# Optimization experiments

Hardware: AMD Instinct MI355X
Metric: run time of the kernel (lower is better)

Reference implementation:

```python
import jax, jax.numpy as jnp
import numpy as np

T, B, D, H = 512, 64, 512, 1024


def setup_inputs() -> dict:
    key = jax.random.key(0)
    ks = jax.random.split(key, 4)
    scale = 1.0 / np.sqrt(D + H)
    return {
        "x": jax.random.normal(ks[0], (T, B, D), dtype=jnp.float32),
        "h0": jnp.zeros((B, H), dtype=jnp.float32),
        "Wz": jax.random.normal(ks[1], (H, D + H), dtype=jnp.float32) * scale,
        "bz": jnp.zeros((H,), dtype=jnp.float32),
        "Wr": jax.random.normal(ks[2], (H, D + H), dtype=jnp.float32) * scale,
        "br": jnp.zeros((H,), dtype=jnp.float32),
        "Wc": jax.random.normal(ks[3], (H, D + H), dtype=jnp.float32) * scale,
        "bc": jnp.zeros((H,), dtype=jnp.float32),
    }


def reference(x, h0, Wz, bz, Wr, br, Wc, bc):
    # x: [T, B, D], h0: [B, H]; weights follow torch Linear layout [out, in].
    def step(h, xt):
        xh = jnp.concatenate([xt, h], axis=-1)           # [B, D+H]
        z = jax.nn.sigmoid(xh @ Wz.T + bz)               # update gate [B, H]
        r = jax.nn.sigmoid(xh @ Wr.T + br)               # reset gate  [B, H]
        xrh = jnp.concatenate([xt, r * h], axis=-1)      # [B, D+H]
        hcand = jnp.tanh(xrh @ Wc.T + bc)                # candidate   [B, H]
        h_new = (1.0 - z) * h + z * hcand
        return h_new, h_new

    _, hist = jax.lax.scan(step, h0, x)                  # hist: [T, B, H]
    return hist
```

## Files before the change

kernel.cpp:

```cpp
#include <hip/hip_runtime.h>
#include <hip/hip_bf16.h>


typedef __attribute__((ext_vector_type(8))) short bf16x8;
typedef __attribute__((ext_vector_type(4))) float f32x4;

#define NWG 128
#define TSTEPS 512

static __device__ __forceinline__ float sigmoidf_fast(float x) {
    return 1.0f / (1.0f + __expf(-x));
}

static __device__ __forceinline__ unsigned short float_to_bf16bits(float f) {
    __hip_bfloat16 b = __float2bfloat16(f);
    unsigned short us;
    __builtin_memcpy(&us, &b, 2);
    return us;
}

static __device__ __forceinline__ void store_coh_u16(void* p, unsigned short v) {
    unsigned vv = v;
    asm volatile("global_store_short %0, %1, off sc0 sc1"
                 :: "v"(p), "v"(vv) : "memory");
}
static __device__ __forceinline__ void store_coh_u32(unsigned* p, unsigned v) {
    asm volatile("global_store_dword %0, %1, off sc0 sc1"
                 :: "v"(p), "v"(v) : "memory");
}

__global__ __launch_bounds__(256) void k_convert_weights(
    const float* __restrict__ Wz, const float* __restrict__ Wr,
    const float* __restrict__ Wc,
    __hip_bfloat16* __restrict__ Wzr, __hip_bfloat16* __restrict__ Wcb)
{
    const long long NW = 1024LL * 1536LL;
    const long long stride = (long long)gridDim.x * blockDim.x;
    for (long long i = (long long)blockIdx.x * blockDim.x + threadIdx.x;
         i < 3 * NW; i += stride) {
        if (i < NW)            Wzr[i] = __float2bfloat16(Wz[i]);
        else if (i < 2 * NW)   Wzr[i] = __float2bfloat16(Wr[i - NW]);
        else                   Wcb[i - 2 * NW] = __float2bfloat16(Wc[i - 2 * NW]);
    }
}

__global__ __launch_bounds__(256) void k_convert_x(
    const float* __restrict__ x, __hip_bfloat16* __restrict__ xb)
{
    const long long N = 512LL * 64LL * 512LL;
    const long long stride = (long long)gridDim.x * blockDim.x;
    for (long long i = (long long)blockIdx.x * blockDim.x + threadIdx.x;
         i < N; i += stride)
        xb[i] = __float2bfloat16(x[i]);
}

__global__ __launch_bounds__(256) void k_init_h(
    const float* __restrict__ h0, __hip_bfloat16* __restrict__ hb)
{
    int i = blockIdx.x * blockDim.x + threadIdx.x;
    hb[i] = __float2bfloat16(h0[i]);
}

__global__ __launch_bounds__(256, 1) void k_gru_persistent(
    const __hip_bfloat16* __restrict__ xb,
    const float* __restrict__ h0,
    __hip_bfloat16* __restrict__ hb_,
    const __hip_bfloat16* __restrict__ Wzr,
    const __hip_bfloat16* __restrict__ Wcb,
    const float* __restrict__ bz, const float* __restrict__ br,
    const float* __restrict__ bc,
    __hip_bfloat16* __restrict__ sb_,
    float* __restrict__ out,
    unsigned* __restrict__ flags)
{
    __shared__ short w1z[64 * 32 * 8];
    __shared__ short w1r[64 * 32 * 8];
    __shared__ short w2c[64 * 32 * 8];
    __shared__ f32x4 red[2][2][64];

    short* hb = (short*)hb_;
    short* sb = (short*)sb_;

    const int g = blockIdx.x;
    const int lane = threadIdx.x & 63;
    const int wave = threadIdx.x >> 6;
    const int r15 = lane & 15;
    const int q = lane >> 4;
    const int kk = q << 3;

    const int dom = g & 3;
    const int wgid = g >> 2;
    const int c0 = wgid * 32;
    const int mt = dom * 16;
    const int tile = wave & 1;
    const int kh = wave >> 1;
    const int jcol = c0 + tile * 16 + r15;
    const int mb = mt + (q << 2);
    const bool owner = (kh == 0);

    unsigned* myline = flags + (dom * 32 + wgid) * 32;
    const unsigned* pollflag = flags + (dom * 32 + (lane & 31)) * 32;

    for (int c = threadIdx.x; c < 64 * 32; c += 256) {
        int row = c & 31, blk = c >> 5;
        bf16x8 vz = *(const bf16x8*)((const short*)Wzr +
                                     (long long)(c0 + row) * 1536 + blk * 8);
        bf16x8 vr = *(const bf16x8*)((const short*)Wzr +
                                     (long long)(1024 + c0 + row) * 1536 + blk * 8);
        bf16x8 vc = *(const bf16x8*)((const short*)Wcb +
                                     (long long)(c0 + row) * 1536 + blk * 8);
        *(bf16x8*)(w1z + (blk * 32 + row) * 8) = vz;
        *(bf16x8*)(w1r + (blk * 32 + row) * 8) = vr;
        *(bf16x8*)(w2c + (blk * 32 + row) * 8) = vc;
    }

    bf16x8 wzh[16], wrh[16], wcs[16];
#pragma unroll
    for (int i = 0; i < 16; ++i) {
        int bk = 64 + kh * 64 + i * 4 + q;
        wzh[i] = *(const bf16x8*)((const short*)Wzr +
                                  (long long)jcol * 1536 + bk * 8);
        wrh[i] = *(const bf16x8*)((const short*)Wzr +
                                  (long long)(1024 + jcol) * 1536 + bk * 8);
        wcs[i] = *(const bf16x8*)((const short*)Wcb +
                                  (long long)jcol * 1536 + bk * 8);
    }

    const float biasZ = bz[jcol];
    const float biasR = br[jcol];
    const float biasC = bc[jcol];

    float hreg[4];
    if (owner) {
#pragma unroll
        for (int v = 0; v < 4; ++v)
            hreg[v] = h0[(mb + v) * 1024 + jcol];
    }
    __syncthreads();

    float zreg[4] = {0.f, 0.f, 0.f, 0.f};

    bf16x8 xc[8];
    {
        const short* Ax0 = (const short*)xb + (mt + r15) * 512 + kh * 256 + kk;
#pragma unroll
        for (int i = 0; i < 8; ++i)
            xc[i] = *(const bf16x8*)(Ax0 + i * 32);
    }

    for (int t = 0; t < TSTEPS; ++t) {
        unsigned f1;
        asm volatile("global_load_dword %0, %1, off sc0 sc1"
                     : "=&v"(f1) : "v"(pollflag) : "memory");

        f32x4 zA = {0.f,0.f,0.f,0.f}, zB = {0.f,0.f,0.f,0.f};
        f32x4 rA = {0.f,0.f,0.f,0.f}, rB = {0.f,0.f,0.f,0.f};
#pragma unroll
        for (int i = 0; i < 8; ++i) {
            int bk = kh * 32 + i * 4 + q;
            bf16x8 wz = *(const bf16x8*)(w1z + (bk * 32 + tile * 16 + r15) * 8);
            bf16x8 wr = *(const bf16x8*)(w1r + (bk * 32 + tile * 16 + r15) * 8);
            if (i & 1) { zB = __builtin_amdgcn_mfma_f32_16x16x32_bf16(xc[i], wz, zB, 0, 0, 0);
                         rB = __builtin_amdgcn_mfma_f32_16x16x32_bf16(xc[i], wr, rB, 0, 0, 0); }
            else       { zA = __builtin_amdgcn_mfma_f32_16x16x32_bf16(xc[i], wz, zA, 0, 0, 0);
                         rA = __builtin_amdgcn_mfma_f32_16x16x32_bf16(xc[i], wr, rA, 0, 0, 0); }
        }
        asm volatile("s_waitcnt vmcnt(0)" ::: "memory");
        __builtin_amdgcn_sched_barrier(0);
        {
            const unsigned gen = (unsigned)(2 * t);
            if (!__all(f1 >= gen)) {
                bool ok;
                do {
                    unsigned fv;
                    asm volatile("global_load_dword %0, %1, off sc0 sc1\n\t"
                                 "s_waitcnt vmcnt(0)"
                                 : "=&v"(fv) : "v"(pollflag) : "memory");
                    ok = (fv >= gen);
                } while (__any(!ok));
            }
        }
        __builtin_amdgcn_sched_barrier(0);

        bf16x8 fr[16], xn[8];
        {
            const short* Ah = hb + (mt + r15) * 1024 + kh * 512 + kk;
            const int tn = (t + 1 < TSTEPS) ? t + 1 : t;
            const short* AxN = (const short*)xb + (long long)tn * 64 * 512 +
                               (mt + r15) * 512 + kh * 256 + kk;
#pragma unroll
            for (int i = 0; i < 16; ++i)
                asm volatile("global_load_dwordx4 %0, %1, off sc0 sc1"
                             : "=&v"(fr[i]) : "v"(Ah + i * 32));
#pragma unroll
            for (int i = 0; i < 8; ++i)
                asm volatile("global_load_dwordx4 %0, %1, off"
                             : "=&v"(xn[i]) : "v"(AxN + i * 32));
            asm volatile("s_waitcnt vmcnt(0)" ::: "memory");
            __builtin_amdgcn_sched_barrier(0);
        }
#pragma unroll
        for (int i = 0; i < 16; ++i) {
            if (i & 1) { zB = __builtin_amdgcn_mfma_f32_16x16x32_bf16(fr[i], wzh[i], zB, 0, 0, 0);
                         rB = __builtin_amdgcn_mfma_f32_16x16x32_bf16(fr[i], wrh[i], rB, 0, 0, 0); }
            else       { zA = __builtin_amdgcn_mfma_f32_16x16x32_bf16(fr[i], wzh[i], zA, 0, 0, 0);
                         rA = __builtin_amdgcn_mfma_f32_16x16x32_bf16(fr[i], wrh[i], rA, 0, 0, 0); }
        }
        {
            f32x4 pz = zA + zB;
            f32x4 pr = rA + rB;
            if (!owner) { red[tile][0][lane] = pz; red[tile][1][lane] = pr; }
            __syncthreads();
            if (owner) {
                f32x4 oz = red[tile][0][lane];
                f32x4 orr = red[tile][1][lane];
#pragma unroll
                for (int v = 0; v < 4; ++v) {
                    zreg[v] = sigmoidf_fast(pz[v] + oz[v] + biasZ);
                    float rv = sigmoidf_fast(pr[v] + orr[v] + biasR);
                    store_coh_u16(sb + (mb + v) * 1024 + jcol,
                                  float_to_bf16bits(rv * hreg[v]));
                }
            }
        }
        asm volatile("s_waitcnt vmcnt(0)" ::: "memory");
        __syncthreads();
        if (threadIdx.x == 0) store_coh_u32(myline, (unsigned)(2 * t + 1));

        unsigned f2;
        asm volatile("global_load_dword %0, %1, off sc0 sc1"
                     : "=&v"(f2) : "v"(pollflag) : "memory");

        f32x4 cA = {0.f,0.f,0.f,0.f}, cB = {0.f,0.f,0.f,0.f};
#pragma unroll
        for (int i = 0; i < 8; ++i) {
            int bk = kh * 32 + i * 4 + q;
            bf16x8 wc = *(const bf16x8*)(w2c + (bk * 32 + tile * 16 + r15) * 8);
            if (i & 1) cB = __builtin_amdgcn_mfma_f32_16x16x32_bf16(xc[i], wc, cB, 0, 0, 0);
            else       cA = __builtin_amdgcn_mfma_f32_16x16x32_bf16(xc[i], wc, cA, 0, 0, 0);
        }
        asm volatile("s_waitcnt vmcnt(0)" ::: "memory");
        __builtin_amdgcn_sched_barrier(0);
        {
            const unsigned gen = (unsigned)(2 * t + 1);
            if (!__all(f2 >= gen)) {
                bool ok;
                do {
                    unsigned fv;
                    asm volatile("global_load_dword %0, %1, off sc0 sc1\n\t"
                                 "s_waitcnt vmcnt(0)"
                                 : "=&v"(fv) : "v"(pollflag) : "memory");
                    ok = (fv >= gen);
                } while (__any(!ok));
            }
        }
        __builtin_amdgcn_sched_barrier(0);

        {
            const short* As = sb + (mt + r15) * 1024 + kh * 512 + kk;
            bf16x8 fs[16];
#pragma unroll
            for (int i = 0; i < 16; ++i)
                asm volatile("global_load_dwordx4 %0, %1, off sc0 sc1"
                             : "=&v"(fs[i]) : "v"(As + i * 32));
            asm volatile("s_waitcnt vmcnt(0)" ::: "memory");
            __builtin_amdgcn_sched_barrier(0);
#pragma unroll
            for (int i = 0; i < 16; ++i) {
                if (i & 1) cB = __builtin_amdgcn_mfma_f32_16x16x32_bf16(fs[i], wcs[i], cB, 0, 0, 0);
                else       cA = __builtin_amdgcn_mfma_f32_16x16x32_bf16(fs[i], wcs[i], cA, 0, 0, 0);
            }
            f32x4 pc = cA + cB;
            if (!owner) red[tile][0][lane] = pc;
            __syncthreads();
            if (owner) {
                f32x4 oc = red[tile][0][lane];
#pragma unroll
                for (int v = 0; v < 4; ++v) {
                    float cv = tanhf(pc[v] + oc[v] + biasC);
                    float h_new = (1.0f - zreg[v]) * hreg[v] + zreg[v] * cv;
                    hreg[v] = h_new;
                    store_coh_u16(hb + (mb + v) * 1024 + jcol,
                                  float_to_bf16bits(h_new));
                }
            }
        }
        asm volatile("s_waitcnt vmcnt(0)" ::: "memory");
        __syncthreads();
        if (threadIdx.x == 0) store_coh_u32(myline, (unsigned)(2 * t + 2));

        if (owner) {
            float* outt = out + (long long)t * 64 * 1024;
#pragma unroll
            for (int v = 0; v < 4; ++v)
                outt[(mb + v) * 1024 + jcol] = hreg[v];
        }
#pragma unroll
        for (int i = 0; i < 8; ++i) xc[i] = xn[i];
    }
}

extern "C" void kernel_launch(void* const* d_in, const int* in_sizes, int n_in,
                              void* d_out, int out_size, void* d_ws, size_t ws_size,
                              hipStream_t stream)
{
    (void)in_sizes; (void)n_in; (void)out_size; (void)ws_size;
    const float* x  = (const float*)d_in[0];
    const float* h0 = (const float*)d_in[1];
    const float* Wz = (const float*)d_in[2];
    const float* bz = (const float*)d_in[3];
    const float* Wr = (const float*)d_in[4];
    const float* br = (const float*)d_in[5];
    const float* Wc = (const float*)d_in[6];
    const float* bc = (const float*)d_in[7];
    float* out = (float*)d_out;

    char* ws = (char*)d_ws;
    __hip_bfloat16* Wzr = (__hip_bfloat16*)(ws);
    __hip_bfloat16* Wcb = (__hip_bfloat16*)(ws + 6291456);
    __hip_bfloat16* xb  = (__hip_bfloat16*)(ws + 9437184);
    __hip_bfloat16* hb  = (__hip_bfloat16*)(ws + 42991616);
    __hip_bfloat16* sb  = (__hip_bfloat16*)(ws + 43122688);
    unsigned*    flags  = (unsigned*)(ws + 43253760);

    k_convert_weights<<<1024, 256, 0, stream>>>(Wz, Wr, Wc, Wzr, Wcb);
    k_convert_x<<<2048, 256, 0, stream>>>(x, xb);
    k_init_h<<<256, 256, 0, stream>>>(h0, hb);
    (void)hipMemsetAsync(flags, 0, 4 * 32 * 32 * sizeof(unsigned), stream);

    k_gru_persistent<<<NWG, 256, 0, stream>>>(
        xb, h0, hb, Wzr, Wcb, bz, br, bc, sb, out, flags);
}
```

Before: 4.285 ms.

## Defer update-gate GEMM to candidate phase and use per-wave completion flags

The update-gate (z) MFMAs move out of the reset-gate phase into the candidate phase. They can then run while waiting for the r*h exchange, which shortens the latency-critical first phase of each timestep. The block-wide __syncthreads plus single per-workgroup flag is replaced by per-owner-wave flags, with 64 slots per domain that pollers read one per lane. This removes two block barriers per step. The flag area doubles in size, and correctness now depends on the per-wave flags ordering the reuse of the shared reduction buffer.

Result: slower. 4.630 ms (+8.1%).

```diff
diff --git a/kernel.cpp b/kernel.cpp
--- a/kernel.cpp
+++ b/kernel.cpp
@@ -98,8 +98,8 @@
     const int mb = mt + (q << 2);
     const bool owner = (kh == 0);
 
-    unsigned* myline = flags + (dom * 32 + wgid) * 32;
-    const unsigned* pollflag = flags + (dom * 32 + (lane & 31)) * 32;
+    unsigned* myslot = flags + (dom * 64 + wgid * 2 + tile) * 32;
+    const unsigned* pollflag = flags + (dom * 64 + lane) * 32;
 
     for (int c = threadIdx.x; c < 64 * 32; c += 256) {
         int row = c & 31, blk = c >> 5;
@@ -138,8 +138,6 @@
     }
     __syncthreads();
 
-    float zreg[4] = {0.f, 0.f, 0.f, 0.f};
-
     bf16x8 xc[8];
     {
         const short* Ax0 = (const short*)xb + (mt + r15) * 512 + kh * 256 + kk;
@@ -153,17 +151,13 @@
         asm volatile("global_load_dword %0, %1, off sc0 sc1"
                      : "=&v"(f1) : "v"(pollflag) : "memory");
 
-        f32x4 zA = {0.f,0.f,0.f,0.f}, zB = {0.f,0.f,0.f,0.f};
         f32x4 rA = {0.f,0.f,0.f,0.f}, rB = {0.f,0.f,0.f,0.f};
 #pragma unroll
         for (int i = 0; i < 8; ++i) {
             int bk = kh * 32 + i * 4 + q;
-            bf16x8 wz = *(const bf16x8*)(w1z + (bk * 32 + tile * 16 + r15) * 8);
             bf16x8 wr = *(const bf16x8*)(w1r + (bk * 32 + tile * 16 + r15) * 8);
-            if (i & 1) { zB = __builtin_amdgcn_mfma_f32_16x16x32_bf16(xc[i], wz, zB, 0, 0, 0);
-                         rB = __builtin_amdgcn_mfma_f32_16x16x32_bf16(xc[i], wr, rB, 0, 0, 0); }
-            else       { zA = __builtin_amdgcn_mfma_f32_16x16x32_bf16(xc[i], wz, zA, 0, 0, 0);
-                         rA = __builtin_amdgcn_mfma_f32_16x16x32_bf16(xc[i], wr, rA, 0, 0, 0); }
+            if (i & 1) rB = __builtin_amdgcn_mfma_f32_16x16x32_bf16(xc[i], wr, rB, 0, 0, 0);
+            else       rA = __builtin_amdgcn_mfma_f32_16x16x32_bf16(xc[i], wr, rA, 0, 0, 0);
         }
         asm volatile("s_waitcnt vmcnt(0)" ::: "memory");
         __builtin_amdgcn_sched_barrier(0);
@@ -201,43 +195,46 @@
         }
 #pragma unroll
         for (int i = 0; i < 16; ++i) {
-            if (i & 1) { zB = __builtin_amdgcn_mfma_f32_16x16x32_bf16(fr[i], wzh[i], zB, 0, 0, 0);
-                         rB = __builtin_amdgcn_mfma_f32_16x16x32_bf16(fr[i], wrh[i], rB, 0, 0, 0); }
-            else       { zA = __builtin_amdgcn_mfma_f32_16x16x32_bf16(fr[i], wzh[i], zA, 0, 0, 0);
-                         rA = __builtin_amdgcn_mfma_f32_16x16x32_bf16(fr[i], wrh[i], rA, 0, 0, 0); }
-        }
-        {
-            f32x4 pz = zA + zB;
+            if (i & 1) rB = __builtin_amdgcn_mfma_f32_16x16x32_bf16(fr[i], wrh[i], rB, 0, 0, 0);
+            else       rA = __builtin_amdgcn_mfma_f32_16x16x32_bf16(fr[i], wrh[i], rA, 0, 0, 0);
+        }
+        {
             f32x4 pr = rA + rB;
-            if (!owner) { red[tile][0][lane] = pz; red[tile][1][lane] = pr; }
+            if (!owner) red[tile][0][lane] = pr;
             __syncthreads();
             if (owner) {
-                f32x4 oz = red[tile][0][lane];
-                f32x4 orr = red[tile][1][lane];
+                f32x4 orr = red[tile][0][lane];
 #pragma unroll
                 for (int v = 0; v < 4; ++v) {
-                    zreg[v] = sigmoidf_fast(pz[v] + oz[v] + biasZ);
                     float rv = sigmoidf_fast(pr[v] + orr[v] + biasR);
                     store_coh_u16(sb + (mb + v) * 1024 + jcol,
                                   float_to_bf16bits(rv * hreg[v]));
                 }
-            }
-        }
-        asm volatile("s_waitcnt vmcnt(0)" ::: "memory");
-        __syncthreads();
-        if (threadIdx.x == 0) store_coh_u32(myline, (unsigned)(2 * t + 1));
+                asm volatile("s_waitcnt vmcnt(0)" ::: "memory");
+                if (lane == 0) store_coh_u32(myslot, (unsigned)(2 * t + 1));
+            }
+        }
 
         unsigned f2;
         asm volatile("global_load_dword %0, %1, off sc0 sc1"
                      : "=&v"(f2) : "v"(pollflag) : "memory");
 
+        f32x4 zA = {0.f,0.f,0.f,0.f}, zB = {0.f,0.f,0.f,0.f};
         f32x4 cA = {0.f,0.f,0.f,0.f}, cB = {0.f,0.f,0.f,0.f};
 #pragma unroll
         for (int i = 0; i < 8; ++i) {
             int bk = kh * 32 + i * 4 + q;
+            bf16x8 wz = *(const bf16x8*)(w1z + (bk * 32 + tile * 16 + r15) * 8);
             bf16x8 wc = *(const bf16x8*)(w2c + (bk * 32 + tile * 16 + r15) * 8);
-            if (i & 1) cB = __builtin_amdgcn_mfma_f32_16x16x32_bf16(xc[i], wc, cB, 0, 0, 0);
-            else       cA = __builtin_amdgcn_mfma_f32_16x16x32_bf16(xc[i], wc, cA, 0, 0, 0);
+            if (i & 1) { zB = __builtin_amdgcn_mfma_f32_16x16x32_bf16(xc[i], wz, zB, 0, 0, 0);
+                         cB = __builtin_amdgcn_mfma_f32_16x16x32_bf16(xc[i], wc, cB, 0, 0, 0); }
+            else       { zA = __builtin_amdgcn_mfma_f32_16x16x32_bf16(xc[i], wz, zA, 0, 0, 0);
+                         cA = __builtin_amdgcn_mfma_f32_16x16x32_bf16(xc[i], wc, cA, 0, 0, 0); }
+        }
+#pragma unroll
+        for (int i = 0; i < 16; ++i) {
+            if (i & 1) zB = __builtin_amdgcn_mfma_f32_16x16x32_bf16(fr[i], wzh[i], zB, 0, 0, 0);
+            else       zA = __builtin_amdgcn_mfma_f32_16x16x32_bf16(fr[i], wzh[i], zA, 0, 0, 0);
         }
         asm volatile("s_waitcnt vmcnt(0)" ::: "memory");
         __builtin_amdgcn_sched_barrier(0);
@@ -270,30 +267,29 @@
                 if (i & 1) cB = __builtin_amdgcn_mfma_f32_16x16x32_bf16(fs[i], wcs[i], cB, 0, 0, 0);
                 else       cA = __builtin_amdgcn_mfma_f32_16x16x32_bf16(fs[i], wcs[i], cA, 0, 0, 0);
             }
+            f32x4 pz = zA + zB;
             f32x4 pc = cA + cB;
-            if (!owner) red[tile][0][lane] = pc;
+            if (!owner) { red[tile][0][lane] = pz; red[tile][1][lane] = pc; }
             __syncthreads();
             if (owner) {
-                f32x4 oc = red[tile][0][lane];
+                f32x4 oz = red[tile][0][lane];
+                f32x4 oc = red[tile][1][lane];
 #pragma unroll
                 for (int v = 0; v < 4; ++v) {
+                    float zv = sigmoidf_fast(pz[v] + oz[v] + biasZ);
                     float cv = tanhf(pc[v] + oc[v] + biasC);
-                    float h_new = (1.0f - zreg[v]) * hreg[v] + zreg[v] * cv;
+                    float h_new = (1.0f - zv) * hreg[v] + zv * cv;
                     hreg[v] = h_new;
                     store_coh_u16(hb + (mb + v) * 1024 + jcol,
                                   float_to_bf16bits(h_new));
                 }
-            }
-        }
-        asm volatile("s_waitcnt vmcnt(0)" ::: "memory");
-        __syncthreads();
-        if (threadIdx.x == 0) store_coh_u32(myline, (unsigned)(2 * t + 2));
-
-        if (owner) {
-            float* outt = out + (long long)t * 64 * 1024;
-#pragma unroll
-            for (int v = 0; v < 4; ++v)
-                outt[(mb + v) * 1024 + jcol] = hreg[v];
+                asm volatile("s_waitcnt vmcnt(0)" ::: "memory");
+                if (lane == 0) store_coh_u32(myslot, (unsigned)(2 * t + 2));
+                float* outt = out + (long long)t * 64 * 1024;
+#pragma unroll
+                for (int v = 0; v < 4; ++v)
+                    outt[(mb + v) * 1024 + jcol] = hreg[v];
+            }
         }
 #pragma unroll
         for (int i = 0; i < 8; ++i) xc[i] = xn[i];
@@ -326,7 +322,7 @@
     k_convert_weights<<<1024, 256, 0, stream>>>(Wz, Wr, Wc, Wzr, Wcb);
     k_convert_x<<<2048, 256, 0, stream>>>(x, xb);
     k_init_h<<<256, 256, 0, stream>>>(h0, hb);
-    (void)hipMemsetAsync(flags, 0, 4 * 32 * 32 * sizeof(unsigned), stream);
+    (void)hipMemsetAsync(flags, 0, 4 * 64 * 32 * sizeof(unsigned), stream);
 
     k_gru_persistent<<<NWG, 256, 0, stream>>>(
         xb, h0, hb, Wzr, Wcb, bz, br, bc, sb, out, flags);
```
